# Kernel optimization log

Measured on AMD Instinct MI355X. Metric: run time of the kernel, lower is better.

The kernel has to match this reference:

```python
import jax, jax.numpy as jnp
import numpy as np

D_MODEL = 1024
NHEAD = 16
D_HEAD = D_MODEL // NHEAD


def setup_inputs() -> dict:
    key = jax.random.key(0)
    ks = jax.random.split(key, 11)
    B, S = 4, 1024
    s = 1.0 / np.sqrt(D_MODEL)
    inp = {
        'q_in': jax.random.normal(ks[0], (B, S, D_MODEL), jnp.float32),
        'k_in': jax.random.normal(ks[1], (B, S, D_MODEL), jnp.float32),
        'v_in': jax.random.normal(ks[2], (B, S, D_MODEL), jnp.float32),
        'Wq': jax.random.normal(ks[3], (D_MODEL, D_MODEL), jnp.float32) * s,
        'bq': jnp.zeros((D_MODEL,), jnp.float32),
        'Wk': jax.random.normal(ks[4], (D_MODEL, D_MODEL), jnp.float32) * s,
        'bk': jnp.zeros((D_MODEL,), jnp.float32),
        'Wv': jax.random.normal(ks[5], (D_MODEL, D_MODEL), jnp.float32) * s,
        'bv': jnp.zeros((D_MODEL,), jnp.float32),
        'Wo': jax.random.normal(ks[6], (D_MODEL, D_MODEL), jnp.float32) * s,
        'bo': jnp.zeros((D_MODEL,), jnp.float32),
    }
    return inp


def reference(q_in, k_in, v_in, Wq, bq, Wk, bk, Wv, bv, Wo, bo):
    B, Sq, _ = q_in.shape
    Sk = k_in.shape[1]
    # Linear projections (torch Linear: x @ W.T + b; here W stored as [in, out])
    Q = q_in @ Wq + bq
    K = k_in @ Wk + bk
    V = v_in @ Wv + bv
    # [B, H, S, Dh]
    Qh = Q.reshape(B, Sq, NHEAD, D_HEAD).transpose(0, 2, 1, 3)
    Kh = K.reshape(B, Sk, NHEAD, D_HEAD).transpose(0, 2, 1, 3)
    Vh = V.reshape(B, Sk, NHEAD, D_HEAD).transpose(0, 2, 1, 3)
    scores = jnp.einsum('bhqd,bhkd->bhqk', Qh, Kh) / jnp.sqrt(jnp.float32(D_HEAD))
    attn_weights = jax.nn.softmax(scores, axis=-1)
    attn = jnp.einsum('bhqk,bhkd->bhqd', attn_weights, Vh)
    attn = attn.transpose(0, 2, 1, 3).reshape(B, Sq, D_MODEL)
    out = attn @ Wo + bo
    return out
```

## Files before the change

### kernel.cpp

```cpp
#include <hip/hip_runtime.h>
#include <hip/hip_bf16.h>
#include <cstdint>
#include <cstddef>

typedef __bf16 bf16_t;
typedef __bf16 bf16x8 __attribute__((ext_vector_type(8)));
typedef __bf16 bf16x4 __attribute__((ext_vector_type(4)));
typedef float f32x4 __attribute__((ext_vector_type(4)));

#define DM 1024
#define NHEAD 16
#define DHEAD 64

#define QSCALE 0.18033688011112042f
#define PSHIFT 4.0f
#define RS 72

__device__ __forceinline__ void gload_lds16(const void* g, void* l) {
    __builtin_amdgcn_global_load_lds(
        (const __attribute__((address_space(1))) void*)g,
        (__attribute__((address_space(3))) void*)l,
        16, 0, 0);
}

__device__ __forceinline__ uint4 cvt8(float4 lo, float4 hi) {
    union { bf16_t b[8]; uint4 u; } o;
    o.b[0] = (bf16_t)lo.x; o.b[1] = (bf16_t)lo.y; o.b[2] = (bf16_t)lo.z; o.b[3] = (bf16_t)lo.w;
    o.b[4] = (bf16_t)hi.x; o.b[5] = (bf16_t)hi.y; o.b[6] = (bf16_t)hi.z; o.b[7] = (bf16_t)hi.w;
    return o.u;
}

__global__ void prep(
    const float* __restrict__ q_in, const float* __restrict__ k_in, const float* __restrict__ v_in,
    bf16_t* __restrict__ Xq, bf16_t* __restrict__ Xk, bf16_t* __restrict__ Xv,
    const float* __restrict__ w0, const float* __restrict__ w1,
    const float* __restrict__ w2, const float* __restrict__ w3,
    bf16_t* __restrict__ t0, bf16_t* __restrict__ t1,
    bf16_t* __restrict__ t2, bf16_t* __restrict__ t3)
{
    __shared__ float tile[32][33];
    int id = blockIdx.x;
    if (id < 6144) {
        int plane = id >> 11;
        int blk = id & 2047;
        const float* x = plane == 0 ? q_in : plane == 1 ? k_in : v_in;
        bf16_t* y      = plane == 0 ? Xq   : plane == 1 ? Xk   : Xv;
        int i = (blk * 256 + threadIdx.x) * 8;
        float4 lo = *(const float4*)&x[i];
        float4 hi = *(const float4*)&x[i + 4];
        *(uint4*)&y[i] = cvt8(lo, hi);
    } else {
        int t = id - 6144;
        int zi = t >> 10;
        int blk = t & 1023;
        const float* w = zi == 0 ? w0 : zi == 1 ? w1 : zi == 2 ? w2 : w3;
        bf16_t* wt     = zi == 0 ? t0 : zi == 1 ? t1 : zi == 2 ? t2 : t3;
        int bx = (blk & 31) * 32;
        int by = (blk >> 5) * 32;
        int tx = threadIdx.x & 31, ty = threadIdx.x >> 5;
        for (int j = 0; j < 32; j += 8)
            tile[ty + j][tx] = w[(size_t)(by + ty + j) * DM + bx + tx];
        __syncthreads();
        for (int j = 0; j < 32; j += 8)
            wt[(size_t)(bx + ty + j) * DM + by + tx] = (bf16_t)tile[tx][ty + j];
    }
}

template <int MODE>
__device__ __forceinline__ void gemm_body(
    const bf16_t* __restrict__ A, const bf16_t* __restrict__ Bt,
    const float* __restrict__ bias, float scale,
    float* __restrict__ Cf, bf16_t* __restrict__ Cb,
    int r0, int c0, bf16_t* AsP, bf16_t* BsP)
{
    const int K = 1024;
    int tid  = threadIdx.x;
    int wave = tid >> 6;
    int lane = tid & 63;
    int quad = lane >> 4;
    int ln   = lane & 15;
    int wr   = wave >> 1;
    int wc   = wave & 1;

    f32x4 acc[4][4];
    for (int rb = 0; rb < 4; rb++)
        for (int cb = 0; cb < 4; cb++)
            acc[rb][cb] = (f32x4){0.f, 0.f, 0.f, 0.f};

    int sr = tid >> 2;
    int sk = (tid & 3) * 8;

    const bf16_t* gA0 = &A[(size_t)(r0 + sr) * K + sk];
    const bf16_t* gA1 = gA0 + (size_t)64 * K;
    const bf16_t* gB0 = &Bt[(size_t)(c0 + sr) * K + sk];
    const bf16_t* gB1 = gB0 + (size_t)64 * K;
    char* lA = (char*)AsP + wave * 1024;
    char* lB = (char*)BsP + wave * 1024;

    for (int k0 = 0; k0 < K; k0 += 32) {
        __syncthreads();
        gload_lds16(gA0 + k0, lA);
        gload_lds16(gA1 + k0, lA + 4096);
        gload_lds16(gB0 + k0, lB);
        gload_lds16(gB1 + k0, lB + 4096);
        __syncthreads();

        bf16x8 af[4], bfv[4];
        for (int rb = 0; rb < 4; rb++)
            af[rb] = *(const bf16x8*)&AsP[(wr * 64 + rb * 16 + ln) * 32 + quad * 8];
        for (int cb = 0; cb < 4; cb++)
            bfv[cb] = *(const bf16x8*)&BsP[(wc * 64 + cb * 16 + ln) * 32 + quad * 8];
        for (int rb = 0; rb < 4; rb++)
            for (int cb = 0; cb < 4; cb++)
                acc[rb][cb] = __builtin_amdgcn_mfma_f32_16x16x32_bf16(af[rb], bfv[cb], acc[rb][cb], 0, 0, 0);
    }

    for (int rb = 0; rb < 4; rb++) {
        for (int cb = 0; cb < 4; cb++) {
            int C = c0 + wc * 64 + cb * 16 + ln;
            for (int r = 0; r < 4; r++) {
                int R = r0 + wr * 64 + rb * 16 + quad * 4 + r;
                float v = acc[rb][cb][r];
                if (MODE == 0) {
                    Cf[(size_t)R * DM + C] = v + bias[C];
                } else if (MODE == 1) {
                    int b = R >> 10, s = R & 1023;
                    int h = C >> 6,  d = C & 63;
                    Cb[(((size_t)b * NHEAD + h) * 1024 + s) * DHEAD + d] =
                        (bf16_t)((v + bias[C]) * scale);
                } else {
                    Cb[((size_t)(C >> 10) * 1024 + R) * 1024 + (C & 1023)] =
                        (bf16_t)(v + bias[R]);
                }
            }
        }
    }
}

__global__ __launch_bounds__(256) void gemm_qkv(
    const bf16_t* __restrict__ Xq, const bf16_t* __restrict__ Xk, const bf16_t* __restrict__ Xv,
    const bf16_t* __restrict__ Wtq, const bf16_t* __restrict__ Wtk, const bf16_t* __restrict__ Wtv,
    const float* __restrict__ bq, const float* __restrict__ bk, const float* __restrict__ bv,
    bf16_t* __restrict__ Qd, bf16_t* __restrict__ Kd, bf16_t* __restrict__ Vt)
{
    __shared__ __align__(16) bf16_t As[128 * 32];
    __shared__ __align__(16) bf16_t Bs[128 * 32];
    int z = blockIdx.z;
    if (z == 0) {
        gemm_body<1>(Xq, Wtq, bq, QSCALE, nullptr, Qd,
                     blockIdx.x * 128, blockIdx.y * 128, As, Bs);
    } else if (z == 1) {
        gemm_body<1>(Xk, Wtk, bk, 1.0f, nullptr, Kd,
                     blockIdx.x * 128, blockIdx.y * 128, As, Bs);
    } else {
        gemm_body<2>(Wtv, Xv, bv, 1.0f, nullptr, Vt,
                     blockIdx.y * 128, blockIdx.x * 128, As, Bs);
    }
}

__global__ __launch_bounds__(256) void gemm_out(
    const bf16_t* __restrict__ At, const bf16_t* __restrict__ Wto,
    const float* __restrict__ bo, float* __restrict__ out)
{
    const int K = 1024;
    __shared__ __align__(16) bf16_t As[64 * 32];
    __shared__ __align__(16) bf16_t Bs[128 * 32];

    int tid  = threadIdx.x;
    int wave = tid >> 6;
    int lane = tid & 63;
    int quad = lane >> 4;
    int ln   = lane & 15;

    int r0 = blockIdx.x * 64;
    int c0 = blockIdx.y * 128;

    f32x4 acc[4][2];
    for (int rb = 0; rb < 4; rb++)
        for (int cb = 0; cb < 2; cb++)
            acc[rb][cb] = (f32x4){0.f, 0.f, 0.f, 0.f};

    int sr = tid >> 2;
    int sk = (tid & 3) * 8;

    const bf16_t* gA0 = At  + (size_t)(r0 + sr) * K + sk;
    const bf16_t* gB0 = Wto + (size_t)(c0 + sr) * K + sk;
    const bf16_t* gB1 = gB0 + (size_t)64 * K;
    char* lA = (char*)As + wave * 1024;
    char* lB = (char*)Bs + wave * 1024;

    for (int k0 = 0; k0 < K; k0 += 32) {
        __syncthreads();
        gload_lds16(gA0 + k0, lA);
        gload_lds16(gB0 + k0, lB);
        gload_lds16(gB1 + k0, lB + 4096);
        __syncthreads();

        bf16x8 af[4], bfv[2];
        for (int rb = 0; rb < 4; rb++)
            af[rb] = *(const bf16x8*)&As[(rb * 16 + ln) * 32 + quad * 8];
        for (int cb = 0; cb < 2; cb++)
            bfv[cb] = *(const bf16x8*)&Bs[(wave * 32 + cb * 16 + ln) * 32 + quad * 8];
        for (int rb = 0; rb < 4; rb++)
            for (int cb = 0; cb < 2; cb++)
                acc[rb][cb] = __builtin_amdgcn_mfma_f32_16x16x32_bf16(af[rb], bfv[cb], acc[rb][cb], 0, 0, 0);
    }

    for (int rb = 0; rb < 4; rb++) {
        for (int cb = 0; cb < 2; cb++) {
            int C = c0 + wave * 32 + cb * 16 + ln;
            float bn = bo[C];
            for (int r = 0; r < 4; r++) {
                int R = r0 + rb * 16 + quad * 4 + r;
                out[(size_t)R * DM + C] = acc[rb][cb][r] + bn;
            }
        }
    }
}

__global__ __launch_bounds__(256) void attn5(
    const bf16_t* __restrict__ Q,
    const bf16_t* __restrict__ K,
    const bf16_t* __restrict__ Vt,
    bf16_t* __restrict__ O)
{
    __shared__ __align__(16) bf16_t Ks[64 * RS];
    __shared__ __align__(16) bf16_t Vs[64 * RS];
    __shared__ __align__(16) bf16_t Ps[4][16 * RS];

    int tid  = threadIdx.x;
    int wave = tid >> 6;
    int lane = tid & 63;
    int quad = lane >> 4;
    int ln   = lane & 15;

    int bh = blockIdx.x;
    int q0w = blockIdx.y * 64 + wave * 16;

    const bf16_t* Qb = Q  + (size_t)bh * 65536;
    const bf16_t* Kb = K  + (size_t)bh * 65536;
    const bf16_t* Vb = Vt + (size_t)bh * 65536;

    int srow = tid >> 3;
    int scol = (tid & 7) * 8;
    const bf16_t* gK0 = Kb + (size_t)srow * 64 + scol;
    const bf16_t* gK1 = gK0 + 32 * 64;
    const bf16_t* gV0 = Vb + (size_t)srow * 1024 + scol;
    const bf16_t* gV1 = gV0 + 32 * 1024;

    bf16x8 aq0 = *(const bf16x8*)&Qb[(size_t)(q0w + ln) * 64 + quad * 8];
    bf16x8 aq1 = *(const bf16x8*)&Qb[(size_t)(q0w + ln) * 64 + 32 + quad * 8];

    uint4 rK0 = *(const uint4*)gK0;
    uint4 rK1 = *(const uint4*)gK1;
    uint4 rV0 = *(const uint4*)gV0;
    uint4 rV1 = *(const uint4*)gV1;

    float l_lane = 0.f;
    f32x4 o_acc[4];
    for (int cb = 0; cb < 4; cb++) o_acc[cb] = (f32x4){0.f, 0.f, 0.f, 0.f};

    bf16_t* Pw = Ps[wave];

    for (int kt = 0; kt < 16; kt++) {
        __syncthreads();
        *(uint4*)&Ks[srow * RS + scol]        = rK0;
        *(uint4*)&Ks[(32 + srow) * RS + scol] = rK1;
        *(uint4*)&Vs[srow * RS + scol]        = rV0;
        *(uint4*)&Vs[(32 + srow) * RS + scol] = rV1;
        __syncthreads();

        if (kt < 15) {
            gK0 += 4096; gK1 += 4096; gV0 += 64; gV1 += 64;
            rK0 = *(const uint4*)gK0;
            rK1 = *(const uint4*)gK1;
            rV0 = *(const uint4*)gV0;
            rV1 = *(const uint4*)gV1;
        }

        f32x4 sc[4];
        for (int kb = 0; kb < 4; kb++) {
            bf16x8 kf0 = *(const bf16x8*)&Ks[(kb * 16 + ln) * RS + quad * 8];
            bf16x8 kf1 = *(const bf16x8*)&Ks[(kb * 16 + ln) * RS + 32 + quad * 8];
            f32x4 a = (f32x4){0.f, 0.f, 0.f, 0.f};
            a = __builtin_amdgcn_mfma_f32_16x16x32_bf16(kf0, aq0, a, 0, 0, 0);
            a = __builtin_amdgcn_mfma_f32_16x16x32_bf16(kf1, aq1, a, 0, 0, 0);
            sc[kb] = a;
        }

        for (int kb = 0; kb < 4; kb++) {
            float p0 = __builtin_amdgcn_exp2f(sc[kb][0] - PSHIFT);
            float p1 = __builtin_amdgcn_exp2f(sc[kb][1] - PSHIFT);
            float p2 = __builtin_amdgcn_exp2f(sc[kb][2] - PSHIFT);
            float p3 = __builtin_amdgcn_exp2f(sc[kb][3] - PSHIFT);
            l_lane += (p0 + p1) + (p2 + p3);
            bf16x4 pk = (bf16x4){(bf16_t)p0, (bf16_t)p1, (bf16_t)p2, (bf16_t)p3};
            *(bf16x4*)&Pw[ln * RS + kb * 16 + quad * 4] = pk;
        }

        for (int kc = 0; kc < 2; kc++) {
            bf16x8 ap = *(const bf16x8*)&Pw[ln * RS + kc * 32 + quad * 8];
            for (int cb = 0; cb < 4; cb++) {
                bf16x8 vf = *(const bf16x8*)&Vs[(cb * 16 + ln) * RS + kc * 32 + quad * 8];
                o_acc[cb] = __builtin_amdgcn_mfma_f32_16x16x32_bf16(ap, vf, o_acc[cb], 0, 0, 0);
            }
        }
    }

    float l = l_lane;
    l += __shfl_xor(l, 16);
    l += __shfl_xor(l, 32);
    float invq[4];
    for (int r = 0; r < 4; r++)
        invq[r] = 1.f / __shfl(l, quad * 4 + r);

    int b = bh >> 4, h = bh & 15;
    for (int cb = 0; cb < 4; cb++) {
        for (int r = 0; r < 4; r++) {
            int q = q0w + quad * 4 + r;
            int d = cb * 16 + ln;
            O[((size_t)b * 1024 + q) * DM + h * 64 + d] = (bf16_t)(o_acc[cb][r] * invq[r]);
        }
    }
}

extern "C" void kernel_launch(void* const* d_in, const int* in_sizes, int n_in,
                              void* d_out, int out_size, void* d_ws, size_t ws_size,
                              hipStream_t stream) {
    const float* q_in = (const float*)d_in[0];
    const float* k_in = (const float*)d_in[1];
    const float* v_in = (const float*)d_in[2];
    const float* Wq   = (const float*)d_in[3];
    const float* bq   = (const float*)d_in[4];
    const float* Wk   = (const float*)d_in[5];
    const float* bk   = (const float*)d_in[6];
    const float* Wv   = (const float*)d_in[7];
    const float* bv   = (const float*)d_in[8];
    const float* Wo   = (const float*)d_in[9];
    const float* bo   = (const float*)d_in[10];

    char* ws = (char*)d_ws;
    const size_t MB = 1024ull * 1024ull;
    bf16_t* Xq  = (bf16_t*)(ws);
    bf16_t* Xk  = (bf16_t*)(ws + 8 * MB);
    bf16_t* Xv  = (bf16_t*)(ws + 16 * MB);
    bf16_t* Wtq = (bf16_t*)(ws + 24 * MB);
    bf16_t* Wtk = (bf16_t*)(ws + 26 * MB);
    bf16_t* Wtv = (bf16_t*)(ws + 28 * MB);
    bf16_t* Wto = (bf16_t*)(ws + 30 * MB);
    bf16_t* Qd  = (bf16_t*)(ws + 32 * MB);
    bf16_t* Kd  = (bf16_t*)(ws + 40 * MB);
    bf16_t* Vt  = (bf16_t*)(ws + 48 * MB);
    bf16_t* At  = Xq;

    prep<<<10240, 256, 0, stream>>>(q_in, k_in, v_in, Xq, Xk, Xv,
                                    Wq, Wk, Wv, Wo, Wtq, Wtk, Wtv, Wto);

    gemm_qkv<<<dim3(32, 8, 3), 256, 0, stream>>>(Xq, Xk, Xv,
                                                 Wtq, Wtk, Wtv, bq, bk, bv, Qd, Kd, Vt);

    attn5<<<dim3(64, 16), 256, 0, stream>>>(Qd, Kd, Vt, At);

    gemm_out<<<dim3(64, 8), 256, 0, stream>>>(At, Wto, bo, (float*)d_out);
}
```

Before: 215.5 us.

## Double-buffer LDS tiles in projection GEMMs to overlap loads with MFMA

Both the QKV and output projection GEMMs now use two LDS buffers. The next K-slice is prefetched with global_load_lds while MFMAs run on the current slice, and one barrier per iteration replaces two. This is meant to hide global-to-LDS latency behind compute. It doubles LDS use per block, which may lower occupancy. The barrier sits at the end of each iteration, so the asynchronous loads must have completed by that point.

```diff
diff --git a/kernel.cpp b/kernel.cpp
--- a/kernel.cpp
+++ b/kernel.cpp
@@ -97,22 +97,36 @@
     char* lA = (char*)AsP + wave * 1024;
     char* lB = (char*)BsP + wave * 1024;
 
+    gload_lds16(gA0, lA);
+    gload_lds16(gA1, lA + 4096);
+    gload_lds16(gB0, lB);
+    gload_lds16(gB1, lB + 4096);
+    __syncthreads();
+
+    int cur = 0;
     for (int k0 = 0; k0 < K; k0 += 32) {
-        __syncthreads();
-        gload_lds16(gA0 + k0, lA);
-        gload_lds16(gA1 + k0, lA + 4096);
-        gload_lds16(gB0 + k0, lB);
-        gload_lds16(gB1 + k0, lB + 4096);
-        __syncthreads();
+        int nxt = cur ^ 1;
+        if (k0 + 32 < K) {
+            int off = nxt * 8192;
+            gload_lds16(gA0 + k0 + 32, lA + off);
+            gload_lds16(gA1 + k0 + 32, lA + off + 4096);
+            gload_lds16(gB0 + k0 + 32, lB + off);
+            gload_lds16(gB1 + k0 + 32, lB + off + 4096);
+        }
+        const bf16_t* Ab = AsP + cur * 4096;
+        const bf16_t* Bb = BsP + cur * 4096;
 
         bf16x8 af[4], bfv[4];
         for (int rb = 0; rb < 4; rb++)
-            af[rb] = *(const bf16x8*)&AsP[(wr * 64 + rb * 16 + ln) * 32 + quad * 8];
+            af[rb] = *(const bf16x8*)&Ab[(wr * 64 + rb * 16 + ln) * 32 + quad * 8];
         for (int cb = 0; cb < 4; cb++)
-            bfv[cb] = *(const bf16x8*)&BsP[(wc * 64 + cb * 16 + ln) * 32 + quad * 8];
+            bfv[cb] = *(const bf16x8*)&Bb[(wc * 64 + cb * 16 + ln) * 32 + quad * 8];
         for (int rb = 0; rb < 4; rb++)
             for (int cb = 0; cb < 4; cb++)
                 acc[rb][cb] = __builtin_amdgcn_mfma_f32_16x16x32_bf16(af[rb], bfv[cb], acc[rb][cb], 0, 0, 0);
+
+        __syncthreads();
+        cur = nxt;
     }
 
     for (int rb = 0; rb < 4; rb++) {
@@ -143,8 +157,8 @@
     const float* __restrict__ bq, const float* __restrict__ bk, const float* __restrict__ bv,
     bf16_t* __restrict__ Qd, bf16_t* __restrict__ Kd, bf16_t* __restrict__ Vt)
 {
-    __shared__ __align__(16) bf16_t As[128 * 32];
-    __shared__ __align__(16) bf16_t Bs[128 * 32];
+    __shared__ __align__(16) bf16_t As[2 * 128 * 32];
+    __shared__ __align__(16) bf16_t Bs[2 * 128 * 32];
     int z = blockIdx.z;
     if (z == 0) {
         gemm_body<1>(Xq, Wtq, bq, QSCALE, nullptr, Qd,
@@ -163,8 +177,8 @@
     const float* __restrict__ bo, float* __restrict__ out)
 {
     const int K = 1024;
-    __shared__ __align__(16) bf16_t As[64 * 32];
-    __shared__ __align__(16) bf16_t Bs[128 * 32];
+    __shared__ __align__(16) bf16_t As[2 * 64 * 32];
+    __shared__ __align__(16) bf16_t Bs[2 * 128 * 32];
 
     int tid  = threadIdx.x;
     int wave = tid >> 6;
@@ -189,21 +203,33 @@
     char* lA = (char*)As + wave * 1024;
     char* lB = (char*)Bs + wave * 1024;
 
+    gload_lds16(gA0, lA);
+    gload_lds16(gB0, lB);
+    gload_lds16(gB1, lB + 4096);
+    __syncthreads();
+
+    int cur = 0;
     for (int k0 = 0; k0 < K; k0 += 32) {
-        __syncthreads();
-        gload_lds16(gA0 + k0, lA);
-        gload_lds16(gB0 + k0, lB);
-        gload_lds16(gB1 + k0, lB + 4096);
-        __syncthreads();
+        int nxt = cur ^ 1;
+        if (k0 + 32 < K) {
+            gload_lds16(gA0 + k0 + 32, lA + nxt * 4096);
+            gload_lds16(gB0 + k0 + 32, lB + nxt * 8192);
+            gload_lds16(gB1 + k0 + 32, lB + nxt * 8192 + 4096);
+        }
+        const bf16_t* Ab = As + cur * 2048;
+        const bf16_t* Bb = Bs + cur * 4096;
 
         bf16x8 af[4], bfv[2];
         for (int rb = 0; rb < 4; rb++)
-            af[rb] = *(const bf16x8*)&As[(rb * 16 + ln) * 32 + quad * 8];
+            af[rb] = *(const bf16x8*)&Ab[(rb * 16 + ln) * 32 + quad * 8];
         for (int cb = 0; cb < 2; cb++)
-            bfv[cb] = *(const bf16x8*)&Bs[(wave * 32 + cb * 16 + ln) * 32 + quad * 8];
+            bfv[cb] = *(const bf16x8*)&Bb[(wave * 32 + cb * 16 + ln) * 32 + quad * 8];
         for (int rb = 0; rb < 4; rb++)
             for (int cb = 0; cb < 2; cb++)
                 acc[rb][cb] = __builtin_amdgcn_mfma_f32_16x16x32_bf16(af[rb], bfv[cb], acc[rb][cb], 0, 0, 0);
+
+        __syncthreads();
+        cur = nxt;
     }
 
     for (int rb = 0; rb < 4; rb++) {
```

After: 208.4 us. 1.03x faster.
